# Kernel tuning notes

Hardware: AMD Instinct MI355X
Metric: run time of the kernel (lower is better)

The kernel has to match this reference:

```python
import jax, jax.numpy as jnp
import numpy as np


def _compute_gradient(f, src, dst, egw):
    # f: [b, c, n] node features; src/dst: [b, e] edge endpoints; egw: [b, e, d]
    # gradient at node src = sum_edges pinvdx * (f[dst] - f[src])
    fT = f.transpose(0, 2, 1)  # b, n, c
    n = fT.shape[1]
    f_dst = jnp.take_along_axis(fT, dst[..., None], axis=1)  # b, e, c
    f_src = jnp.take_along_axis(fT, src[..., None], axis=1)  # b, e, c
    msg = egw[..., :, None] * (f_dst - f_src)[..., None, :]  # b, e, d, c
    b, e, d, c = msg.shape

    def seg(m, s):
        return jax.ops.segment_sum(m.reshape(e, d * c), s, num_segments=n)

    grad = jax.vmap(seg)(msg, src)  # b, n, d*c
    return grad.transpose(0, 2, 1)  # b, d*c, n


def _forward(x, t, nodes, node_weights, edge_gradient_weights, modes, sp_L,
             fc0_w, fc0_b, Wc, Ws, W0, ws_w, ws_b, gws_w, gws_b,
             fc1_w, fc1_b, fc2_w, fc2_b, directed_edges):
    D = nodes.shape[-1]
    # Fourier bases: modes [k,d,w] scaled by sp_L [d,w]
    temp = jnp.einsum('bxd,kdw->bxkw', nodes, modes * sp_L)
    bc, bs = jnp.cos(temp), jnp.sin(temp)
    b0 = jnp.ones(temp[:, :, :1, :].shape, temp.dtype)
    nw = node_weights[:, :, None, :]
    wbc, wbs, wb0 = bc * nw, bs * nw, b0 * nw

    x_value = x[:, :, :D]
    h = jnp.concatenate([x, t], -1) @ fc0_w + fc0_b  # b, n, c
    h = h.transpose(0, 2, 1)  # b, c, n

    src = directed_edges[..., 0]
    dst = directed_edges[..., 1]
    nlayers = ws_w.shape[0]
    for i in range(nlayers):
        # spectral convolution (real Fourier transform on scattered points)
        xc = jnp.einsum('bcx,bxkw->bckw', h, wbc)
        xs = -jnp.einsum('bcx,bxkw->bckw', h, wbs)
        x0 = jnp.einsum('bcx,bxkw->bckw', h, wb0)
        fc_ = jnp.einsum('bikw,iokw->bokw', xc, Wc[i]) - jnp.einsum('bikw,iokw->bokw', xs, Ws[i])
        fs_ = jnp.einsum('bikw,iokw->bokw', xs, Wc[i]) + jnp.einsum('bikw,iokw->bokw', xc, Ws[i])
        f0_ = jnp.einsum('bikw,iokw->bokw', x0, W0[i])
        x1 = (jnp.einsum('bokw,bxkw->box', f0_, b0)
              + 2.0 * jnp.einsum('bokw,bxkw->box', fc_, bc)
              - 2.0 * jnp.einsum('bokw,bxkw->box', fs_, bs))
        # pointwise linear (Conv1d kernel size 1)
        x2 = jnp.einsum('oc,bcx->box', ws_w[i], h) + ws_b[i][None, :, None]
        # gradient operator + softsign + Conv1d
        g = _compute_gradient(h, src, dst, edge_gradient_weights)  # b, d*c, n
        g = g / (1.0 + jnp.abs(g))  # softsign
        x3 = jnp.einsum('oc,bcx->box', gws_w[i], g) + gws_b[i][None, :, None]
        h = x1 + x2 + x3
        if i != nlayers - 1:
            h = jax.nn.gelu(h, approximate=False)

    h = h.transpose(0, 2, 1)  # b, n, c
    h = jax.nn.gelu(h @ fc1_w + fc1_b, approximate=False)
    h = h @ fc2_w + fc2_b
    return x_value + t * h


def setup_inputs() -> dict:
    B, N, E = 2, 20000, 100000
    D, W, K, C, L, FC, OUT = 3, 1, 128, 128, 3, 128, 3
    key = jax.random.key(0)
    k = jax.random.split(key, 16)
    x = jax.random.normal(k[0], (B, N, D), jnp.float32)
    t = jax.random.uniform(k[1], (B, N, 1), jnp.float32)
    node_mask = jnp.ones((B, N, 1), jnp.int32)
    nodes = jax.random.uniform(k[2], (B, N, D), jnp.float32)
    node_weights = jax.random.uniform(k[3], (B, N, W), jnp.float32) / N
    directed_edges = jax.random.randint(k[4], (B, E, 2), 0, N)
    edge_gradient_weights = jax.random.normal(k[5], (B, E, D), jnp.float32)
    modes = jax.random.normal(k[6], (K, D, W), jnp.float32) * (2.0 * np.pi)
    sp_L = jnp.ones((D, W), jnp.float32)
    fc0_w = jax.random.normal(k[7], (D + 1, C), jnp.float32) * 0.1
    fc0_b = jnp.zeros((C,), jnp.float32)
    scale = 1.0 / (C * C)
    Wc = jax.random.uniform(k[8], (L, C, C, K, W), jnp.float32) * scale
    Ws = jax.random.uniform(k[9], (L, C, C, K, W), jnp.float32) * scale
    W0 = jax.random.uniform(k[10], (L, C, C, 1, W), jnp.float32) * scale
    ws_w = jax.random.normal(k[11], (L, C, C), jnp.float32) * 0.05
    ws_b = jnp.zeros((L, C), jnp.float32)
    gws_w = jax.random.normal(k[12], (L, C, D * C), jnp.float32) * 0.05
    gws_b = jnp.zeros((L, C), jnp.float32)
    fc1_w = jax.random.normal(k[13], (C, FC), jnp.float32) * 0.05
    fc1_b = jnp.zeros((FC,), jnp.float32)
    fc2_w = jax.random.normal(k[14], (FC, OUT), jnp.float32) * 0.05
    fc2_b = jnp.zeros((OUT,), jnp.float32)
    return dict(x=x, t=t, node_mask=node_mask, nodes=nodes, node_weights=node_weights,
                directed_edges=directed_edges, edge_gradient_weights=edge_gradient_weights,
                modes=modes, sp_L=sp_L, fc0_w=fc0_w, fc0_b=fc0_b, Wc=Wc, Ws=Ws, W0=W0,
                ws_w=ws_w, ws_b=ws_b, gws_w=gws_w, gws_b=gws_b,
                fc1_w=fc1_w, fc1_b=fc1_b, fc2_w=fc2_w, fc2_b=fc2_b)


def reference(x, t, node_mask, nodes, node_weights, directed_edges, edge_gradient_weights,
              modes, sp_L, fc0_w, fc0_b, Wc, Ws, W0, ws_w, ws_b, gws_w, gws_b,
              fc1_w, fc1_b, fc2_w, fc2_b):
    del node_mask  # unpacked but unused in the original forward
    return _forward(x, t, nodes, node_weights, edge_gradient_weights, modes, sp_L,
                    fc0_w, fc0_b, Wc, Ws, W0, ws_w, ws_b, gws_w, gws_b,
                    fc1_w, fc1_b, fc2_w, fc2_b, directed_edges)
```

## Files before the change

kernel.cpp:

```cpp
#include <hip/hip_runtime.h>
#include <math.h>

#define BB 2
#define NN 20000
#define EE 100000
#define DD 3
#define KK 128
#define CC 128
#define LL 3
#define FCC 128
#define GJ (DD*CC)
#define KR 768
#define NP 20096
#define NCHK 157
#define G1CH 40
#define G1N 512

typedef __attribute__((ext_vector_type(8))) short bf16x8;
typedef __attribute__((ext_vector_type(4))) float f32x4;

__device__ inline unsigned short f2bf(float f) {
  unsigned int u = __float_as_uint(f);
  u += 0x7fffu + ((u >> 16) & 1u);
  return (unsigned short)(u >> 16);
}
__device__ inline float bf2f(unsigned short u) {
  return __uint_as_float(((unsigned int)u) << 16);
}

__device__ float d_nw[BB*NN];
__device__ __align__(16) unsigned short d_stackT[(size_t)BB*NP*KR];
__device__ __align__(16) unsigned short d_bcT[(size_t)BB*KK*NP];
__device__ __align__(16) unsigned short d_bsT[(size_t)BB*KK*NP];
__device__ __align__(16) unsigned short d_hTwT[(size_t)BB*CC*NP];
__device__ __align__(16) unsigned short d_Amatb[BB*CC*KR];
__device__ __align__(16) unsigned short d_fc1wb[FCC*CC];
__device__ __align__(16) float d_part[(size_t)BB*4*G1CH*2*64*64];
__device__ float d_xc[BB*CC*KK];
__device__ float d_xs[BB*CC*KK];
__device__ float d_x0p[BB*NCHK*CC];
__device__ float d_fcp[BB*CC*8*KK];
__device__ float d_fsp[BB*CC*8*KK];
__device__ float d_bias[BB*CC];
__device__ int d_cnt[BB*NN];
__device__ int d_cursor[BB*NN];
__device__ int d_off[BB*(NN+1)];
__device__ __align__(16) float4 d_erec[(size_t)BB*EE];

__global__ __launch_bounds__(128) void k_basis(const float* __restrict__ nodes,
                                               const float* __restrict__ nodew,
                                               const float* __restrict__ modes,
                                               const float* __restrict__ spL) {
  int bn = blockIdx.x;
  int k  = threadIdx.x;
  int b = bn / NN, n = bn % NN;
  float x0 = nodes[bn*3+0], x1 = nodes[bn*3+1], x2 = nodes[bn*3+2];
  float tmp = x0*modes[k*3+0]*spL[0] + x1*modes[k*3+1]*spL[1] + x2*modes[k*3+2]*spL[2];
  float cv = cosf(tmp), sv = sinf(tmp);
  size_t row = (size_t)(b*NP + n);
  d_stackT[row*KR + k]       = f2bf(cv);
  d_stackT[row*KR + 128 + k] = f2bf(sv);
  if (k == 0) d_nw[bn] = nodew[bn];
}

__global__ __launch_bounds__(256) void k_basisT() {
  __shared__ unsigned short t1[32][136];
  __shared__ unsigned short t2[32][136];
  int blk = blockIdx.x;
  int nt = blk % 628, b = blk / 628;
  int n0 = nt*32;
  int tid = threadIdx.x;
  int kl = tid & 127, ng = tid >> 7;
  for (int nn = ng; nn < 32; nn += 2) {
    int n = n0 + nn;
    unsigned short cv = 0, sv = 0;
    if (n < NN) {
      const unsigned short* sp = d_stackT + ((size_t)(b*NP + n))*KR;
      cv = sp[kl]; sv = sp[128 + kl];
    }
    t1[nn][kl] = cv;
    t2[nn][kl] = sv;
  }
  __syncthreads();
  int nl = tid & 31, kg = tid >> 5;
  for (int k = kg; k < 128; k += 8) {
    d_bcT[((size_t)(b*KK + k))*NP + n0 + nl] = t1[nl][k];
    d_bsT[((size_t)(b*KK + k))*NP + n0 + nl] = t2[nl][k];
  }
}

__global__ __launch_bounds__(256) void k_csr_zero() {
  int tid = blockIdx.x*256 + threadIdx.x;
  if (tid < BB*NN) { d_cnt[tid] = 0; d_cursor[tid] = 0; }
}

__global__ __launch_bounds__(256) void k_csr_count(const int* __restrict__ edges) {
  int e = blockIdx.x*256 + threadIdx.x;
  if (e >= BB*EE) return;
  int b = e / EE;
  int src = edges[e*2 + 0];
  atomicAdd(&d_cnt[b*NN + src], 1);
}

__global__ __launch_bounds__(1024) void k_csr_scan() {
  int b = blockIdx.x;
  __shared__ int sdata[1024];
  __shared__ int carry_s;
  int tid = threadIdx.x;
  if (tid == 0) carry_s = 0;
  __syncthreads();
  for (int chunk = 0; chunk < 20; ++chunk) {
    int i = chunk*1024 + tid;
    int v = (i < NN) ? d_cnt[b*NN + i] : 0;
    sdata[tid] = v;
    __syncthreads();
    for (int s = 1; s < 1024; s <<= 1) {
      int tv = (tid >= s) ? sdata[tid - s] : 0;
      __syncthreads();
      sdata[tid] += tv;
      __syncthreads();
    }
    int excl = carry_s + sdata[tid] - v;
    if (i < NN) d_off[b*(NN+1) + i] = excl;
    __syncthreads();
    if (tid == 1023) carry_s += sdata[1023];
    __syncthreads();
  }
  if (tid == 0) d_off[b*(NN+1) + NN] = carry_s;
}

__global__ __launch_bounds__(256) void k_csr_scatter(const int* __restrict__ edges,
                                                     const float* __restrict__ egw) {
  int e = blockIdx.x*256 + threadIdx.x;
  if (e >= BB*EE) return;
  int b = e / EE;
  int src = edges[e*2 + 0];
  int dst = edges[e*2 + 1];
  int pos = atomicAdd(&d_cursor[b*NN + src], 1);
  d_erec[(size_t)b*EE + d_off[b*(NN+1) + src] + pos] =
      make_float4(__int_as_float(dst), egw[e*3+0], egw[e*3+1], egw[e*3+2]);
}

__global__ __launch_bounds__(256) void k_h0(const float* __restrict__ x,
                                            const float* __restrict__ t,
                                            const float* __restrict__ w,
                                            const float* __restrict__ bias) {
  int tid = blockIdx.x*256 + threadIdx.x;
  int c = tid & 127;
  int bn = tid >> 7;
  int b = bn / NN, n = bn % NN;
  const float* xv = x + bn*3;
  float acc = bias[c] + xv[0]*w[c] + xv[1]*w[CC+c] + xv[2]*w[2*CC+c]
            + t[bn]*w[3*CC+c];
  d_stackT[((size_t)(b*NP + n))*KR + 256 + c] = f2bf(acc);
}

__global__ __launch_bounds__(256) void k_hT0() {
  __shared__ unsigned short t[128][136];
  int chunk = blockIdx.x;
  int b = blockIdx.y;
  int n0 = chunk*128;
  int tid = threadIdx.x;
  int cl = tid & 127, ng = tid >> 7;
  for (int nn = ng; nn < 128; nn += 2) {
    int n = n0 + nn;
    unsigned short v = 0;
    if (n < NN) {
      float hv = bf2f(d_stackT[((size_t)(b*NP + n))*KR + 256 + cl]);
      v = f2bf(hv * d_nw[b*NN + n]);
    }
    t[nn][cl] = v;
  }
  __syncthreads();
  int nl = tid & 31, cg = tid >> 5;
  for (int c = cg; c < 128; c += 8)
    for (int nn2 = 0; nn2 < 128; nn2 += 32)
      d_hTwT[((size_t)(b*CC + c))*NP + n0 + nn2 + nl] = t[nn2 + nl][c];
}

__global__ __launch_bounds__(256) void k_gemm1m() {
  __shared__ unsigned short Ash[2][64*40];
  __shared__ unsigned short Bch[2][64*40];
  __shared__ unsigned short Bsh[2][64*40];
  int chunk = blockIdx.x;
  int quad  = blockIdx.y;
  int b     = blockIdx.z;
  int ch = quad >> 1, kh = quad & 1;
  int tid = threadIdx.x, lane = tid & 63, wid = tid >> 6;
  int q = lane >> 4, m = lane & 15;
  f32x4 accC[4], accS[4];
  #pragma unroll
  for (int j = 0; j < 4; j++) { accC[j] = (f32x4){0.f,0.f,0.f,0.f}; accS[j] = (f32x4){0.f,0.f,0.f,0.f}; }
  const unsigned short* Ab  = d_hTwT + ((size_t)(b*CC + ch*64))*NP;
  const unsigned short* Bcp = d_bcT + ((size_t)(b*KK + kh*64))*NP;
  const unsigned short* Bsp = d_bsT + ((size_t)(b*KK + kh*64))*NP;
  int n0 = chunk*G1N;

#define G1STAGE(nb, d) { \
    int row_ = tid >> 2; int e8_ = (tid & 3)*8; \
    if ((nb) < NP) { \
      *(uint4*)&Ash[d][row_*40 + e8_] = *(const uint4*)(Ab  + (size_t)row_*NP + (nb) + e8_); \
      *(uint4*)&Bch[d][row_*40 + e8_] = *(const uint4*)(Bcp + (size_t)row_*NP + (nb) + e8_); \
      *(uint4*)&Bsh[d][row_*40 + e8_] = *(const uint4*)(Bsp + (size_t)row_*NP + (nb) + e8_); \
    } else { \
      uint4 z_ = make_uint4(0,0,0,0); \
      *(uint4*)&Ash[d][row_*40 + e8_] = z_; \
      *(uint4*)&Bch[d][row_*40 + e8_] = z_; \
      *(uint4*)&Bsh[d][row_*40 + e8_] = z_; \
    } }

  G1STAGE(n0, 0)
  int cur = 0;
  for (int s = 0; s < G1N/32; s++) {
    __syncthreads();
    if (s + 1 < G1N/32) G1STAGE(n0 + (s+1)*32, cur ^ 1)
    bf16x8 a = *(const bf16x8*)&Ash[cur][(wid*16 + m)*40 + q*8];
    #pragma unroll
    for (int kt = 0; kt < 4; kt++) {
      bf16x8 bcf = *(const bf16x8*)&Bch[cur][(kt*16 + m)*40 + q*8];
      accC[kt] = __builtin_amdgcn_mfma_f32_16x16x32_bf16(a, bcf, accC[kt], 0, 0, 0);
      bf16x8 bsf = *(const bf16x8*)&Bsh[cur][(kt*16 + m)*40 + q*8];
      accS[kt] = __builtin_amdgcn_mfma_f32_16x16x32_bf16(a, bsf, accS[kt], 0, 0, 0);
    }
    cur ^= 1;
  }
#undef G1STAGE

  float* base = d_part + ((size_t)(b*4 + quad)*G1CH + chunk)*2*4096;
  #pragma unroll
  for (int kt = 0; kt < 4; kt++)
    #pragma unroll
    for (int r = 0; r < 4; r++) {
      int c = wid*16 + q*4 + r;
      int k = kt*16 + m;
      base[c*64 + k]        =  accC[kt][r];
      base[4096 + c*64 + k] = -accS[kt][r];
    }
}

__global__ __launch_bounds__(256) void k_grad_csr() {
  int bn = blockIdx.x*2 + (threadIdx.x >> 7);
  int c = threadIdx.x & 127;
  int b = bn / NN, n = bn % NN;
  int beg = d_off[b*(NN+1) + n];
  int end = d_off[b*(NN+1) + n + 1];
  const float4* rp = d_erec + (size_t)b*EE;
  const unsigned short* hb = d_stackT + (size_t)b*NP*KR + 256 + c;
  float a0 = 0.f, a1 = 0.f, a2 = 0.f;
  float sw0 = 0.f, sw1 = 0.f, sw2 = 0.f;
  int p = beg;
  for (; p + 4 <= end; p += 4) {
    float4 r1 = rp[p], r2 = rp[p+1], r3 = rp[p+2], r4 = rp[p+3];
    float f1 = bf2f(hb[(size_t)__float_as_int(r1.x)*KR]);
    float f2 = bf2f(hb[(size_t)__float_as_int(r2.x)*KR]);
    float f3 = bf2f(hb[(size_t)__float_as_int(r3.x)*KR]);
    float f4 = bf2f(hb[(size_t)__float_as_int(r4.x)*KR]);
    a0 += r1.y*f1 + r2.y*f2 + r3.y*f3 + r4.y*f4;
    a1 += r1.z*f1 + r2.z*f2 + r3.z*f3 + r4.z*f4;
    a2 += r1.w*f1 + r2.w*f2 + r3.w*f3 + r4.w*f4;
    sw0 += r1.y + r2.y + r3.y + r4.y;
    sw1 += r1.z + r2.z + r3.z + r4.z;
    sw2 += r1.w + r2.w + r3.w + r4.w;
  }
  for (; p < end; ++p) {
    float4 r1 = rp[p];
    float f1 = bf2f(hb[(size_t)__float_as_int(r1.x)*KR]);
    a0 += r1.y*f1; a1 += r1.z*f1; a2 += r1.w*f1;
    sw0 += r1.y; sw1 += r1.z; sw2 += r1.w;
  }
  float fs = bf2f(hb[(size_t)n*KR]);
  a0 -= sw0*fs; a1 -= sw1*fs; a2 -= sw2*fs;
  unsigned short* gp = d_stackT + ((size_t)(b*NP + n))*KR + 384;
  gp[c]        = f2bf(a0/(1.f + fabsf(a0)));
  gp[CC + c]   = f2bf(a1/(1.f + fabsf(a1)));
  gp[2*CC + c] = f2bf(a2/(1.f + fabsf(a2)));
}

__global__ __launch_bounds__(256) void k_red_x0() {
  int blk = blockIdx.x;
  if (blk < 256) {
    int tid = blk*256 + threadIdx.x;
    int k = tid & 127;
    int c = (tid >> 7) & 127;
    int arr = (tid >> 14) & 1;
    int b = tid >> 15;
    int ch = c >> 6, cl = c & 63;
    int kh = k >> 6, kl = k & 63;
    int quad = ch*2 + kh;
    const float* p = d_part + ((size_t)(b*4 + quad)*G1CH)*2*4096 + arr*4096 + cl*64 + kl;
    float acc = 0.f;
    for (int t = 0; t < G1CH; t++) acc += p[(size_t)t*2*4096];
    if (arr == 0) d_xc[(b*CC + c)*KK + k] = acc;
    else          d_xs[(b*CC + c)*KK + k] = acc;
  } else {
    int bc = blk - 256;
    int chunk = bc % NCHK, b = bc / NCHK;
    int tid = threadIdx.x;
    int c = tid >> 1, half = tid & 1;
    const unsigned short* p = d_hTwT + ((size_t)(b*CC + c))*NP + chunk*128 + half*64;
    float acc = 0.f;
    #pragma unroll
    for (int i = 0; i < 8; i++) {
      ushort4 v0 = *(const ushort4*)&p[i*8];
      ushort4 v1 = *(const ushort4*)&p[i*8 + 4];
      acc += bf2f(v0.x) + bf2f(v0.y) + bf2f(v0.z) + bf2f(v0.w)
           + bf2f(v1.x) + bf2f(v1.y) + bf2f(v1.z) + bf2f(v1.w);
    }
    __shared__ float red[128][2];
    red[c][half] = acc;
    __syncthreads();
    if (half == 0) d_x0p[(b*NCHK + chunk)*CC + c] = red[c][0] + red[c][1];
  }
}

__global__ __launch_bounds__(128) void k_spec(const float* __restrict__ Wc,
                                              const float* __restrict__ Ws, int l) {
  int bo = blockIdx.x;
  int ch = blockIdx.y;
  int b = bo >> 7;
  int o = bo & 127;
  int k = threadIdx.x;
  int i0 = ch*16;
  const float* wcp = Wc + ((size_t)(l*CC + i0)*CC + o)*KK + k;
  const float* wsp = Ws + ((size_t)(l*CC + i0)*CC + o)*KK + k;
  float fc = 0.f, fs = 0.f;
  #pragma unroll 4
  for (int j = 0; j < 16; j++) {
    int i = i0 + j;
    float xcv = d_xc[(b*CC + i)*KK + k];
    float xsv = d_xs[(b*CC + i)*KK + k];
    float wcv = wcp[(size_t)j*CC*KK];
    float wsv = wsp[(size_t)j*CC*KK];
    fc += xcv*wcv - xsv*wsv;
    fs += xsv*wcv + xcv*wsv;
  }
  d_fcp[((size_t)bo*8 + ch)*KK + k] = fc;
  d_fsp[((size_t)bo*8 + ch)*KK + k] = fs;
}

__global__ __launch_bounds__(128) void k_bA_f0(const float* __restrict__ wsw,
                                               const float* __restrict__ gwsw,
                                               const float* __restrict__ W0,
                                               const float* __restrict__ wsb,
                                               const float* __restrict__ gwsb, int l) {
  int blk = blockIdx.x;
  int t = threadIdx.x;
  if (blk < 256) {
    int bo = blk;
    int b = bo >> 7, o = bo & 127;
    float fc = 0.f, fs = 0.f;
    #pragma unroll
    for (int ch = 0; ch < 8; ch++) {
      fc += d_fcp[((size_t)bo*8 + ch)*KK + t];
      fs += d_fsp[((size_t)bo*8 + ch)*KK + t];
    }
    unsigned short* dst = d_Amatb + (size_t)bo*KR;
    dst[t]       = f2bf( 2.f*fc);
    dst[128 + t] = f2bf(-2.f*fs);
    dst[256 + t] = f2bf(wsw[(l*CC + o)*CC + t]);
    #pragma unroll
    for (int j = 0; j < 3; j++)
      dst[384 + j*128 + t] = f2bf(gwsw[(size_t)(l*CC + o)*GJ + j*128 + t]);
  } else {
    int b = blk - 256;
    int o = t;
    __shared__ float sx[CC];
    float xv = 0.f;
    for (int p = 0; p < NCHK; p++) xv += d_x0p[(b*NCHK + p)*CC + o];
    sx[o] = xv;
    __syncthreads();
    float acc = 0.f;
    for (int i = 0; i < CC; i++) acc += sx[i]*W0[(l*CC + i)*CC + o];
    d_bias[b*CC + o] = acc + wsb[l*CC + o] + gwsb[l*CC + o];
  }
}

__global__ __launch_bounds__(128) void k_fc1w(const float* __restrict__ fc1w) {
  int c = blockIdx.x;
  int o2 = threadIdx.x;
  d_fc1wb[o2*CC + c] = f2bf(fc1w[c*FCC + o2]);
}

__global__ __launch_bounds__(512) void k_mfma(int koff, int K,
                                              const unsigned short* __restrict__ W, size_t wstride,
                                              const float* __restrict__ bias, int bias_stride,
                                              int gelu, int aux,
                                              const float* __restrict__ xvec,
                                              const float* __restrict__ tvec,
                                              const float* __restrict__ fc2w,
                                              const float* __restrict__ fc2b,
                                              float* __restrict__ outp) {
  __shared__ unsigned short As[2][64*72];
  __shared__ unsigned short Bs[2][128*72];
  __shared__ float sh_nw[64];
  int b = blockIdx.z;
  int n_base = blockIdx.x*64;
  int tid = threadIdx.x;
  int lane = tid & 63, wid = tid >> 6;
  int wr = wid >> 1, wc = wid & 1;
  int q = lane >> 4, m = lane & 15;

  f32x4 acc[4];
  #pragma unroll
  for (int j = 0; j < 4; j++) acc[j] = (f32x4){0.f,0.f,0.f,0.f};

  const unsigned short* Wb = W + (size_t)b*wstride;
  const unsigned short* Ab = d_stackT + (size_t)b*NP*KR + koff;

#define STAGE(k0, d) { \
    { int rowA = tid >> 3; int e8A = (tid & 7)*8; \
      *(uint4*)&As[d][rowA*72 + e8A] = *(const uint4*)(Ab + (size_t)(n_base + rowA)*KR + (k0) + e8A); } \
    _Pragma("unroll") \
    for (int i_ = 0; i_ < 2; i_++) { \
      int idx_ = tid + i_*512; int rowB = idx_ >> 3; int e8B = (idx_ & 7)*8; \
      *(uint4*)&Bs[d][rowB*72 + e8B] = *(const uint4*)(Wb + (size_t)rowB*K + (k0) + e8B); } }

  STAGE(0, 0)
  int cur = 0;
  for (int k0 = 0; k0 < K; k0 += 64) {
    __syncthreads();
    if (k0 + 64 < K) STAGE(k0 + 64, cur ^ 1)
    bf16x8 a0 = *(const bf16x8*)&As[cur][(wr*16 + m)*72 + q*8];
    bf16x8 a1 = *(const bf16x8*)&As[cur][(wr*16 + m)*72 + 32 + q*8];
    __builtin_amdgcn_s_setprio(1);
    #pragma unroll
    for (int ot = 0; ot < 4; ot++) {
      bf16x8 b0 = *(const bf16x8*)&Bs[cur][(wc*64 + ot*16 + m)*72 + q*8];
      acc[ot] = __builtin_amdgcn_mfma_f32_16x16x32_bf16(a0, b0, acc[ot], 0, 0, 0);
      bf16x8 b1 = *(const bf16x8*)&Bs[cur][(wc*64 + ot*16 + m)*72 + 32 + q*8];
      acc[ot] = __builtin_amdgcn_mfma_f32_16x16x32_bf16(a1, b1, acc[ot], 0, 0, 0);
    }
    __builtin_amdgcn_s_setprio(0);
    cur ^= 1;
  }
#undef STAGE

  __syncthreads();
  unsigned short* Ep = &As[0][0];
  if (tid < 64) {
    int n = n_base + tid;
    sh_nw[tid] = (aux && n < NN) ? d_nw[b*NN + n] : 0.f;
  }
  const float* bp = bias + (size_t)b*bias_stride;
  int lrow = wr*16 + q*4;
  #pragma unroll
  for (int ot = 0; ot < 4; ot++) {
    int o = wc*64 + ot*16 + m;
    float bvv = bp[o];
    #pragma unroll
    for (int r = 0; r < 4; r++) {
      float v = acc[ot][r] + bvv;
      if (gelu) v = 0.5f*v*(1.f + erff(v*0.70710678118f));
      Ep[(lrow + r)*132 + o] = f2bf(v);
    }
  }
  __syncthreads();
  if (aux) {
    {
      int row = tid >> 3;
      int c16 = (tid & 7)*16;
      int n = n_base + row;
      if (n < NN) {
        uint4 v0 = *(uint4*)&Ep[row*132 + c16];
        uint4 v1 = *(uint4*)&Ep[row*132 + c16 + 8];
        unsigned short* dst = d_stackT + ((size_t)(b*NP + n))*KR + 256;
        *(uint4*)&dst[c16]     = v0;
        *(uint4*)&dst[c16 + 8] = v1;
      }
    }
    {
      int o = tid >> 2;
      int j0 = (tid & 3)*16;
      unsigned short tmp[16];
      #pragma unroll
      for (int j = 0; j < 16; j++) {
        float hv = bf2f(Ep[(j0 + j)*132 + o]);
        tmp[j] = f2bf(hv * sh_nw[j0 + j]);
      }
      unsigned short* dst = d_hTwT + ((size_t)(b*CC + o))*NP + n_base + j0;
      *(uint4*)&dst[0] = *(uint4*)&tmp[0];
      *(uint4*)&dst[8] = *(uint4*)&tmp[8];
    }
  } else {
    int row = tid >> 3, j = tid & 7;
    int n = n_base + row;
    float p0 = 0.f, p1 = 0.f, p2 = 0.f;
    int o0 = j*16;
    #pragma unroll
    for (int oo = 0; oo < 16; oo++) {
      float uv = bf2f(Ep[row*132 + o0 + oo]);
      p0 += uv*fc2w[(o0+oo)*3 + 0];
      p1 += uv*fc2w[(o0+oo)*3 + 1];
      p2 += uv*fc2w[(o0+oo)*3 + 2];
    }
    #pragma unroll
    for (int s2 = 1; s2 < 8; s2 <<= 1) {
      p0 += __shfl_xor(p0, s2);
      p1 += __shfl_xor(p1, s2);
      p2 += __shfl_xor(p2, s2);
    }
    if (j == 0 && n < NN) {
      int bn = b*NN + n;
      float tv = tvec[bn];
      outp[bn*3 + 0] = xvec[bn*3 + 0] + tv*(p0 + fc2b[0]);
      outp[bn*3 + 1] = xvec[bn*3 + 1] + tv*(p1 + fc2b[1]);
      outp[bn*3 + 2] = xvec[bn*3 + 2] + tv*(p2 + fc2b[2]);
    }
  }
}

extern "C" void kernel_launch(void* const* d_in, const int* in_sizes, int n_in,
                              void* d_out, int out_size, void* d_ws, size_t ws_size,
                              hipStream_t stream) {
  const float* x     = (const float*)d_in[0];
  const float* t     = (const float*)d_in[1];
  const float* nodes = (const float*)d_in[3];
  const float* nodew = (const float*)d_in[4];
  const int*   edges = (const int*)d_in[5];
  const float* egw   = (const float*)d_in[6];
  const float* modes = (const float*)d_in[7];
  const float* spL   = (const float*)d_in[8];
  const float* fc0w  = (const float*)d_in[9];
  const float* fc0b  = (const float*)d_in[10];
  const float* Wc    = (const float*)d_in[11];
  const float* Ws    = (const float*)d_in[12];
  const float* W0    = (const float*)d_in[13];
  const float* wsw   = (const float*)d_in[14];
  const float* wsb   = (const float*)d_in[15];
  const float* gwsw  = (const float*)d_in[16];
  const float* gwsb  = (const float*)d_in[17];
  const float* fc1w  = (const float*)d_in[18];
  const float* fc1b  = (const float*)d_in[19];
  const float* fc2w  = (const float*)d_in[20];
  const float* fc2b  = (const float*)d_in[21];
  float* out = (float*)d_out;

  unsigned short* d_Amatb_p; hipGetSymbolAddress((void**)&d_Amatb_p, HIP_SYMBOL(d_Amatb));
  unsigned short* d_fc1wb_p; hipGetSymbolAddress((void**)&d_fc1wb_p, HIP_SYMBOL(d_fc1wb));
  float* d_bias_p;  hipGetSymbolAddress((void**)&d_bias_p,  HIP_SYMBOL(d_bias));

  hipLaunchKernelGGL(k_basis, dim3(BB*NN), dim3(128), 0, stream, nodes, nodew, modes, spL);
  hipLaunchKernelGGL(k_basisT, dim3(628*BB), dim3(256), 0, stream);
  hipLaunchKernelGGL(k_h0, dim3(BB*NN*CC/256), dim3(256), 0, stream, x, t, fc0w, fc0b);
  hipLaunchKernelGGL(k_hT0, dim3(NCHK, BB), dim3(256), 0, stream);
  hipLaunchKernelGGL(k_fc1w, dim3(CC), dim3(FCC), 0, stream, fc1w);
  hipLaunchKernelGGL(k_csr_zero, dim3((BB*NN + 255)/256), dim3(256), 0, stream);
  hipLaunchKernelGGL(k_csr_count, dim3((BB*EE + 255)/256), dim3(256), 0, stream, edges);
  hipLaunchKernelGGL(k_csr_scan, dim3(BB), dim3(1024), 0, stream);
  hipLaunchKernelGGL(k_csr_scatter, dim3((BB*EE + 255)/256), dim3(256), 0, stream, edges, egw);

  for (int l = 0; l < LL; l++) {
    hipLaunchKernelGGL(k_gemm1m, dim3(G1CH, 4, BB), dim3(256), 0, stream);
    hipLaunchKernelGGL(k_grad_csr, dim3(BB*NN/2), dim3(256), 0, stream);
    hipLaunchKernelGGL(k_red_x0, dim3(256 + NCHK*BB), dim3(256), 0, stream);
    hipLaunchKernelGGL(k_spec, dim3(BB*CC, 8), dim3(128), 0, stream, Wc, Ws, l);
    hipLaunchKernelGGL(k_bA_f0, dim3(BB*CC + BB), dim3(128), 0, stream,
                       wsw, gwsw, W0, wsb, gwsb, l);
    hipLaunchKernelGGL(k_mfma, dim3(NP/64, 1, BB), dim3(512), 0, stream,
                       0, KR, d_Amatb_p, (size_t)CC*KR, d_bias_p, CC,
                       (l != LL-1) ? 1 : 0, 1,
                       (const float*)nullptr, (const float*)nullptr,
                       (const float*)nullptr, (const float*)nullptr, (float*)nullptr);
  }

  hipLaunchKernelGGL(k_mfma, dim3(NP/64, 1, BB), dim3(512), 0, stream,
                     256, CC, d_fc1wb_p, (size_t)0, fc1b, 0, 1, 0,
                     x, t, fc2w, fc2b, out);
}
```

Before: 488.1 us.

## Halve k_mfma row tile and write transposed weighted output from registers

Shrinks the k_mfma tile from 64 to 32 node rows with 256-thread blocks, which doubles the grid so more workgroups can run across CUs. The node-weighted transposed output d_hTwT is now written straight from MFMA accumulator registers as 4-element packed stores, instead of a second pass through shared memory with a strided transpose read. The setprio hints are also removed. In exchange, each block reloads the full 128-row weight tile for only half as many rows, which doubles the B-operand traffic per node.

```diff
diff --git a/kernel.cpp b/kernel.cpp
--- a/kernel.cpp
+++ b/kernel.cpp
@@ -381,7 +381,7 @@
   d_fc1wb[o2*CC + c] = f2bf(fc1w[c*FCC + o2]);
 }
 
-__global__ __launch_bounds__(512) void k_mfma(int koff, int K,
+__global__ __launch_bounds__(256) void k_mfma(int koff, int K,
                                               const unsigned short* __restrict__ W, size_t wstride,
                                               const float* __restrict__ bias, int bias_stride,
                                               int gelu, int aux,
@@ -390,11 +390,10 @@
                                               const float* __restrict__ fc2w,
                                               const float* __restrict__ fc2b,
                                               float* __restrict__ outp) {
-  __shared__ unsigned short As[2][64*72];
+  __shared__ unsigned short As[2][32*72];
   __shared__ unsigned short Bs[2][128*72];
-  __shared__ float sh_nw[64];
   int b = blockIdx.z;
-  int n_base = blockIdx.x*64;
+  int n_base = blockIdx.x*32;
   int tid = threadIdx.x;
   int lane = tid & 63, wid = tid >> 6;
   int wr = wid >> 1, wc = wid & 1;
@@ -411,8 +410,8 @@
     { int rowA = tid >> 3; int e8A = (tid & 7)*8; \
       *(uint4*)&As[d][rowA*72 + e8A] = *(const uint4*)(Ab + (size_t)(n_base + rowA)*KR + (k0) + e8A); } \
     _Pragma("unroll") \
-    for (int i_ = 0; i_ < 2; i_++) { \
-      int idx_ = tid + i_*512; int rowB = idx_ >> 3; int e8B = (idx_ & 7)*8; \
+    for (int i_ = 0; i_ < 4; i_++) { \
+      int idx_ = tid + i_*256; int rowB = idx_ >> 3; int e8B = (idx_ & 7)*8; \
       *(uint4*)&Bs[d][rowB*72 + e8B] = *(const uint4*)(Wb + (size_t)rowB*K + (k0) + e8B); } }
 
   STAGE(0, 0)
@@ -422,7 +421,6 @@
     if (k0 + 64 < K) STAGE(k0 + 64, cur ^ 1)
     bf16x8 a0 = *(const bf16x8*)&As[cur][(wr*16 + m)*72 + q*8];
     bf16x8 a1 = *(const bf16x8*)&As[cur][(wr*16 + m)*72 + 32 + q*8];
-    __builtin_amdgcn_s_setprio(1);
     #pragma unroll
     for (int ot = 0; ot < 4; ot++) {
       bf16x8 b0 = *(const bf16x8*)&Bs[cur][(wc*64 + ot*16 + m)*72 + q*8];
@@ -430,56 +428,51 @@
       bf16x8 b1 = *(const bf16x8*)&Bs[cur][(wc*64 + ot*16 + m)*72 + 32 + q*8];
       acc[ot] = __builtin_amdgcn_mfma_f32_16x16x32_bf16(a1, b1, acc[ot], 0, 0, 0);
     }
-    __builtin_amdgcn_s_setprio(0);
     cur ^= 1;
   }
 #undef STAGE
 
   __syncthreads();
   unsigned short* Ep = &As[0][0];
-  if (tid < 64) {
-    int n = n_base + tid;
-    sh_nw[tid] = (aux && n < NN) ? d_nw[b*NN + n] : 0.f;
-  }
   const float* bp = bias + (size_t)b*bias_stride;
   int lrow = wr*16 + q*4;
+  int nb4 = n_base + lrow;
+  float nw4[4];
+  #pragma unroll
+  for (int r = 0; r < 4; r++)
+    nw4[r] = (aux && nb4 + r < NN) ? d_nw[b*NN + nb4 + r] : 0.f;
   #pragma unroll
   for (int ot = 0; ot < 4; ot++) {
     int o = wc*64 + ot*16 + m;
     float bvv = bp[o];
+    float vals[4];
     #pragma unroll
     for (int r = 0; r < 4; r++) {
       float v = acc[ot][r] + bvv;
       if (gelu) v = 0.5f*v*(1.f + erff(v*0.70710678118f));
+      vals[r] = v;
       Ep[(lrow + r)*132 + o] = f2bf(v);
+    }
+    if (aux) {
+      ushort4 pk;
+      pk.x = f2bf(vals[0]*nw4[0]);
+      pk.y = f2bf(vals[1]*nw4[1]);
+      pk.z = f2bf(vals[2]*nw4[2]);
+      pk.w = f2bf(vals[3]*nw4[3]);
+      *(ushort4*)&d_hTwT[((size_t)(b*CC + o))*NP + nb4] = pk;
     }
   }
   __syncthreads();
   if (aux) {
-    {
-      int row = tid >> 3;
-      int c16 = (tid & 7)*16;
-      int n = n_base + row;
-      if (n < NN) {
-        uint4 v0 = *(uint4*)&Ep[row*132 + c16];
-        uint4 v1 = *(uint4*)&Ep[row*132 + c16 + 8];
-        unsigned short* dst = d_stackT + ((size_t)(b*NP + n))*KR + 256;
-        *(uint4*)&dst[c16]     = v0;
-        *(uint4*)&dst[c16 + 8] = v1;
-      }
-    }
-    {
-      int o = tid >> 2;
-      int j0 = (tid & 3)*16;
-      unsigned short tmp[16];
-      #pragma unroll
-      for (int j = 0; j < 16; j++) {
-        float hv = bf2f(Ep[(j0 + j)*132 + o]);
-        tmp[j] = f2bf(hv * sh_nw[j0 + j]);
-      }
-      unsigned short* dst = d_hTwT + ((size_t)(b*CC + o))*NP + n_base + j0;
-      *(uint4*)&dst[0] = *(uint4*)&tmp[0];
-      *(uint4*)&dst[8] = *(uint4*)&tmp[8];
+    int row = tid >> 3;
+    int c16 = (tid & 7)*16;
+    int n = n_base + row;
+    if (n < NN) {
+      uint4 v0 = *(uint4*)&Ep[row*132 + c16];
+      uint4 v1 = *(uint4*)&Ep[row*132 + c16 + 8];
+      unsigned short* dst = d_stackT + ((size_t)(b*NP + n))*KR + 256;
+      *(uint4*)&dst[c16]     = v0;
+      *(uint4*)&dst[c16 + 8] = v1;
     }
   } else {
     int row = tid >> 3, j = tid & 7;
@@ -535,9 +528,9 @@
   const float* fc2b  = (const float*)d_in[21];
   float* out = (float*)d_out;
 
-  unsigned short* d_Amatb_p; hipGetSymbolAddress((void**)&d_Amatb_p, HIP_SYMBOL(d_Amatb));
-  unsigned short* d_fc1wb_p; hipGetSymbolAddress((void**)&d_fc1wb_p, HIP_SYMBOL(d_fc1wb));
-  float* d_bias_p;  hipGetSymbolAddress((void**)&d_bias_p,  HIP_SYMBOL(d_bias));
+  unsigned short* d_Amatb_p; (void)hipGetSymbolAddress((void**)&d_Amatb_p, HIP_SYMBOL(d_Amatb));
+  unsigned short* d_fc1wb_p; (void)hipGetSymbolAddress((void**)&d_fc1wb_p, HIP_SYMBOL(d_fc1wb));
+  float* d_bias_p;  (void)hipGetSymbolAddress((void**)&d_bias_p,  HIP_SYMBOL(d_bias));
 
   hipLaunchKernelGGL(k_basis, dim3(BB*NN), dim3(128), 0, stream, nodes, nodew, modes, spL);
   hipLaunchKernelGGL(k_basisT, dim3(628*BB), dim3(256), 0, stream);
@@ -556,14 +549,14 @@
     hipLaunchKernelGGL(k_spec, dim3(BB*CC, 8), dim3(128), 0, stream, Wc, Ws, l);
     hipLaunchKernelGGL(k_bA_f0, dim3(BB*CC + BB), dim3(128), 0, stream,
                        wsw, gwsw, W0, wsb, gwsb, l);
-    hipLaunchKernelGGL(k_mfma, dim3(NP/64, 1, BB), dim3(512), 0, stream,
+    hipLaunchKernelGGL(k_mfma, dim3(NP/32, 1, BB), dim3(256), 0, stream,
                        0, KR, d_Amatb_p, (size_t)CC*KR, d_bias_p, CC,
                        (l != LL-1) ? 1 : 0, 1,
                        (const float*)nullptr, (const float*)nullptr,
                        (const float*)nullptr, (const float*)nullptr, (float*)nullptr);
   }
 
-  hipLaunchKernelGGL(k_mfma, dim3(NP/64, 1, BB), dim3(512), 0, stream,
+  hipLaunchKernelGGL(k_mfma, dim3(NP/32, 1, BB), dim3(256), 0, stream,
                      256, CC, d_fc1wb_p, (size_t)0, fc1b, 0, 1, 0,
                      x, t, fc2w, fc2b, out);
 }
```

Measured after the change: 504.3 us. 3.3% more time.
